# Performance work log

Hardware: AMD Instinct MI355X
Metric: run time of the kernel (lower is better)

## Reference

```python
import jax, jax.numpy as jnp
import numpy as np

NUM_HEADS = 8
POOL = 4  # kq_downscale kernel/stride (spatial)
B, S, H, W, C = 32, 8, 32, 32, 128
TOTAL_KEY_DEPTH = 512
VAL_FILTERS = 128
OUT_FILTERS = 64


def _avg_pool(x):
    # tf.nn.avg_pool3d with kernel/stride [1,1,4,4,1], SAME padding (dims divide evenly)
    win = (1, 1, POOL, POOL, 1)
    s = jax.lax.reduce_window(x, 0.0, jax.lax.add, win, win, 'SAME')
    return s / (POOL * POOL)


def _conv2d(x, w, b):
    # TimeDistributed Conv2D, same padding. x: (B,S,H,W,Cin), w: (kh,kw,Cin,Cout)
    Bx, Sx, Hx, Wx, Cx = x.shape
    y = jax.lax.conv_general_dilated(
        x.reshape(Bx * Sx, Hx, Wx, Cx), w, (1, 1), 'SAME',
        dimension_numbers=('NHWC', 'HWIO', 'NHWC'))
    return y.reshape(Bx, Sx, Hx, Wx, -1) + b


def _rel_emb(length_q, length_k, max_rel, table):
    # _generate_relative_positions_embeddings
    rk = jnp.arange(length_k)
    rq = rk[-length_q:]
    idx = jnp.clip(rk[None, :] - rq[:, None], -max_rel, max_rel) + max_rel
    return table[idx]  # (Lq, Lk, depth)


def setup_inputs() -> dict:
    key = jax.random.key(0)
    ks = jax.random.split(key, 11)
    qk_in = (H // POOL) * (W // POOL) * C          # 8*8*128 = 8192
    d_vh = H * W * VAL_FILTERS // NUM_HEADS         # 16384 per-head value depth
    d_kh = TOTAL_KEY_DEPTH // NUM_HEADS             # 64
    return {
        'inputs': jax.random.normal(ks[0], (B, 1, H, W, C), jnp.float32),
        'k_antecedent': jax.random.normal(ks[1], (B, S, H, W, C), jnp.float32),
        'v_antecedent': jax.random.normal(ks[2], (B, S, H, W, C), jnp.float32),
        'w_q': jax.random.normal(ks[3], (qk_in, TOTAL_KEY_DEPTH), jnp.float32) * 0.02,
        'w_k': jax.random.normal(ks[4], (qk_in, TOTAL_KEY_DEPTH), jnp.float32) * 0.02,
        'conv_v_w': jax.random.normal(ks[5], (3, 3, C, VAL_FILTERS), jnp.float32) * 0.02,
        'conv_v_b': jnp.zeros((VAL_FILTERS,), jnp.float32),
        'conv_o_w': jax.random.normal(ks[6], (3, 3, VAL_FILTERS, OUT_FILTERS), jnp.float32) * 0.02,
        'conv_o_b': jnp.zeros((OUT_FILTERS,), jnp.float32),
        'table_k': jax.random.normal(ks[7], (S, d_kh), jnp.float32) * 0.05,
        'table_v': jax.random.normal(ks[8], (S, d_vh), jnp.float32) * 0.05,
    }


def reference(inputs, k_antecedent, v_antecedent, w_q, w_k,
              conv_v_w, conv_v_b, conv_o_w, conv_o_b, table_k, table_v):
    Bx, Sx, Hx, Wx, Cx = v_antecedent.shape
    nh = NUM_HEADS
    max_rel = Sx // 2 - 1  # attn_factor_reduc/2 - 1

    # downscale + flatten q/k antecedents
    q_a = _avg_pool(inputs).reshape(Bx, 1, -1)
    k_a = _avg_pool(k_antecedent).reshape(Bx, Sx, -1)
    q = q_a @ w_q                   # (B,1,Dk)
    k = k_a @ w_k                   # (B,S,Dk)
    v = _conv2d(v_antecedent, conv_v_w, conv_v_b).reshape(Bx, Sx, -1)  # (B,S,Dv)

    def split(x):  # (B,L,D) -> (B,h,L,D/h)
        Bz, L, D = x.shape
        return x.reshape(Bz, L, nh, D // nh).transpose(0, 2, 1, 3)

    q, k, v = split(q), split(k), split(v)
    q = q * (q.shape[-1] ** -0.5)

    # relative-position logits: _relative_attention_inner(q, k, z_k, transpose=True)
    z_k = _rel_emb(1, Sx, max_rel, table_k)  # (1,S,dkh)
    logits = jnp.einsum('bhqd,bhkd->bhqk', q, k) + jnp.einsum('bhqd,qkd->bhqk', q, z_k)
    weights = jax.nn.softmax(logits, axis=-1)  # (B,h,1,S)

    # relative values: _relative_attention_inner(weights, v, z_v, transpose=False)
    z_v = _rel_emb(1, Sx, max_rel, table_v)  # (1,S,dvh)
    x = jnp.einsum('bhqk,bhkd->bhqd', weights, v) + jnp.einsum('bhqk,qkd->bhqd', weights, z_v)

    # combine heads, restore spatial shape, output conv
    x = x.transpose(0, 2, 1, 3).reshape(Bx, 1, Hx, Wx, -1)  # (B,1,H,W,Fv)
    out = _conv2d(x, conv_o_w, conv_o_b)                     # (B,1,H,W,Fo)
    return out
```

## Files before the change

kernel.cpp:

```cpp
#include <hip/hip_runtime.h>
#include <hip/hip_bf16.h>

typedef __hip_bfloat16 bf16;
typedef __attribute__((ext_vector_type(8))) short bf16x8;
typedef __attribute__((ext_vector_type(4))) float f32x4;

constexpr int B_ = 32, S_ = 8, H_ = 32, W_ = 32, C_ = 128;
constexpr int NH_ = 8, KD_ = 512, DKH_ = 64, VF_ = 128, OF_ = 64;
constexpr int QKIN_ = 8192;

static __device__ __forceinline__ short bfbits(float f) {
    bf16 h = __float2bfloat16(f);
    short s;
    __builtin_memcpy(&s, &h, 2);
    return s;
}
static __device__ __forceinline__ unsigned int packbf2(float a, float b) {
    return ((unsigned int)(unsigned short)bfbits(b) << 16) | (unsigned short)bfbits(a);
}


static __device__ __forceinline__ void dev_pool4(const float* __restrict__ in,
                                                 short* __restrict__ out, int idx) {
    int c4 = (idx & 31) * 4;
    int pw = (idx >> 5) & 7;
    int ph = (idx >> 8) & 7;
    int img = idx >> 11;
    const float* p = in + (((size_t)img * H_ + ph * 4) * W_ + pw * 4) * C_ + c4;
    float4 s = {0.f, 0.f, 0.f, 0.f};
#pragma unroll
    for (int dy = 0; dy < 4; ++dy)
#pragma unroll
        for (int dx = 0; dx < 4; ++dx) {
            float4 v = *reinterpret_cast<const float4*>(p + (dy * W_ + dx) * C_);
            s.x += v.x; s.y += v.y; s.z += v.z; s.w += v.w;
        }
    uint2 pk;
    pk.x = packbf2(s.x * 0.0625f, s.y * 0.0625f);
    pk.y = packbf2(s.z * 0.0625f, s.w * 0.0625f);
    *reinterpret_cast<uint2*>(out + (size_t)img * QKIN_ + (ph * 8 + pw) * 128 + c4) = pk;
}

static __device__ __forceinline__ void dev_wT(const float* __restrict__ w,
                                              short* __restrict__ wT, int local,
                                              float (*t)[65]) {
    int k0 = (local >> 3) * 64, n0 = (local & 7) * 64;
    int col = threadIdx.x & 63, r4 = threadIdx.x >> 6;
#pragma unroll
    for (int i = 0; i < 16; ++i) {
        int kr = i * 4 + r4;
        t[kr][col] = w[(size_t)(k0 + kr) * KD_ + n0 + col];
    }
    __syncthreads();
    int n = threadIdx.x >> 3, kg = threadIdx.x & 7;
#pragma unroll
    for (int half = 0; half < 2; ++half) {
        int nn = n + half * 32;
        short v[8];
#pragma unroll
        for (int j = 0; j < 8; ++j) v[j] = bfbits(t[kg * 8 + j][nn]);
        *reinterpret_cast<bf16x8*>(wT + (size_t)(n0 + nn) * QKIN_ + k0 + kg * 8) =
            *reinterpret_cast<bf16x8*>(v);
    }
}

static __device__ __forceinline__ void dev_wtrans(const float* __restrict__ in,
                                                  short* __restrict__ out, int idx,
                                                  int CO) {
    int tap = idx / (128 * CO);
    int rem = idx % (128 * CO);
    int co = rem / 128;
    int ci = rem & 127;
    out[idx] = bfbits(in[((size_t)tap * 128 + ci) * CO + co]);
}

constexpr int PB_ZERO  = 144;
constexpr int PB_POOLI = PB_ZERO + 256;
constexpr int PB_POOLK = PB_POOLI + 2048;
constexpr int PB_WTQ   = PB_POOLK + 1024;
constexpr int PB_WTK   = PB_WTQ + 1024;
constexpr int PB_WV    = PB_WTK + 576;
constexpr int PB_WO    = PB_WV + 288;

__global__ __launch_bounds__(256) void k_prep(
    const float* __restrict__ inp, const float* __restrict__ k_ant,
    const float* __restrict__ w_q, const float* __restrict__ w_k,
    const float* __restrict__ cvw, const float* __restrict__ cow,
    float* __restrict__ qk_zero, short* __restrict__ q_a, short* __restrict__ k_a,
    short* __restrict__ wqT, short* __restrict__ wkT,
    short* __restrict__ wvT, short* __restrict__ woT) {
    __shared__ float t[64][65];
    int bx = blockIdx.x;
    if (bx < PB_ZERO) {
        int i = (bx * 256 + threadIdx.x) * 4;
        float4 z = {0.f, 0.f, 0.f, 0.f};
        *reinterpret_cast<float4*>(qk_zero + i) = z;
    } else if (bx < PB_POOLI) {
        dev_pool4(inp, q_a, (bx - PB_ZERO) * 256 + threadIdx.x);
    } else if (bx < PB_POOLK) {
        dev_pool4(k_ant, k_a, (bx - PB_POOLI) * 256 + threadIdx.x);
    } else if (bx < PB_WTK) {
        if (bx < PB_WTQ)
            dev_wT(w_q, wqT, bx - PB_POOLK, t);
        else
            dev_wT(w_k, wkT, bx - PB_WTQ, t);
    } else if (bx < PB_WV) {
        dev_wtrans(cvw, wvT, (bx - PB_WTK) * 256 + threadIdx.x, 128);
    } else {
        dev_wtrans(cow, woT, (bx - PB_WV) * 256 + threadIdx.x, 64);
    }
}

__global__ __launch_bounds__(256) void k_gemm2(
    const short* __restrict__ qa, const short* __restrict__ ka,
    const short* __restrict__ wqTp, const short* __restrict__ wkTp,
    float* __restrict__ qo, float* __restrict__ ko) {
    int wave = threadIdx.x >> 6, lane = threadIdx.x & 63;
    int quad = lane >> 4, l15 = lane & 15;
    int id = blockIdx.x;
    const short* A;
    const short* WT;
    float* out;
    int m0, rem;
    if (id < 64) {
        A = qa; WT = wqTp; out = qo; m0 = 0; rem = id;
    } else {
        id -= 64;
        A = ka; WT = wkTp; out = ko;
        m0 = (id >> 6) * 32; rem = id & 63;
    }
    int n0 = (rem & 3) * 128 + wave * 32;
    int k0 = (rem >> 2) * 512;
    f32x4 acc[2][2];
#pragma unroll
    for (int mt = 0; mt < 2; ++mt)
#pragma unroll
        for (int nt = 0; nt < 2; ++nt) acc[mt][nt] = (f32x4){0.f, 0.f, 0.f, 0.f};
    const short* a0p = A + (size_t)(m0 + l15) * QKIN_;
    const short* a1p = a0p + 16 * QKIN_;
    const short* b0p = WT + (size_t)(n0 + l15) * QKIN_;
    const short* b1p = b0p + 16 * QKIN_;
    for (int kk = k0 + quad * 8; kk < k0 + 512; kk += 32) {
        bf16x8 a0 = *reinterpret_cast<const bf16x8*>(a0p + kk);
        bf16x8 a1 = *reinterpret_cast<const bf16x8*>(a1p + kk);
        bf16x8 b0 = *reinterpret_cast<const bf16x8*>(b0p + kk);
        bf16x8 b1 = *reinterpret_cast<const bf16x8*>(b1p + kk);
        acc[0][0] = __builtin_amdgcn_mfma_f32_16x16x32_bf16(a0, b0, acc[0][0], 0, 0, 0);
        acc[0][1] = __builtin_amdgcn_mfma_f32_16x16x32_bf16(a0, b1, acc[0][1], 0, 0, 0);
        acc[1][0] = __builtin_amdgcn_mfma_f32_16x16x32_bf16(a1, b0, acc[1][0], 0, 0, 0);
        acc[1][1] = __builtin_amdgcn_mfma_f32_16x16x32_bf16(a1, b1, acc[1][1], 0, 0, 0);
    }
#pragma unroll
    for (int mt = 0; mt < 2; ++mt)
#pragma unroll
        for (int nt = 0; nt < 2; ++nt)
#pragma unroll
            for (int reg = 0; reg < 4; ++reg)
                atomicAdd(&out[(size_t)(m0 + mt * 16 + quad * 4 + reg) * KD_ +
                               n0 + nt * 16 + l15],
                          acc[mt][nt][reg]);
}

__global__ __launch_bounds__(256) void k_convv_mfma(
    const float* __restrict__ v_ant, const short* __restrict__ wvT,
    const float* __restrict__ bias, const float* __restrict__ tbv,
    const float* __restrict__ q, const float* __restrict__ kmat,
    const float* __restrict__ tbk, short* __restrict__ x) {
    __shared__ short strip[6 * 34 * 136];
    __shared__ float w8s[8];
    int b = blockIdx.x >> 3, h = blockIdx.x & 7;
    int y0 = 4 * h;
    if (threadIdx.x < 64) {
        int d = threadIdx.x;
        float qv = q[(size_t)b * KD_ + h * DKH_ + d];
        float lg[8];
        float m = -1e30f;
#pragma unroll
        for (int s = 0; s < 8; ++s) {
            int zi = (s < 4) ? 0 : (s - 4);
            float kv = kmat[((size_t)b * S_ + s) * KD_ + h * DKH_ + d] + tbk[zi * DKH_ + d];
            float p = qv * kv * 0.125f;
#pragma unroll
            for (int msk = 1; msk < 64; msk <<= 1) p += __shfl_xor(p, msk);
            lg[s] = p;
            m = fmaxf(m, p);
        }
        float sum = 0.f;
#pragma unroll
        for (int s = 0; s < 8; ++s) {
            lg[s] = expf(lg[s] - m);
            sum += lg[s];
        }
        if (d == 0) {
            float inv = 1.f / sum;
#pragma unroll
            for (int s = 0; s < 8; ++s) w8s[s] = lg[s] * inv;
        }
    }
    for (int i = threadIdx.x; i < 384; i += 256) {
        int r = i >> 6, remz = i & 63;
        int side = remz >> 5, cg = remz & 31;
        uint2 z = {0u, 0u};
        *reinterpret_cast<uint2*>(&strip[(r * 34 + side * 33) * 136 + cg * 4]) = z;
    }
    __syncthreads();
    float w8[8];
#pragma unroll
    for (int kk = 0; kk < 8; ++kk) w8[kk] = w8s[kk];
    for (int i = threadIdx.x; i < 6 * 1024; i += 256) {
        int r = i >> 10, rem = i & 1023;
        int yimg = y0 - 1 + r;
        float4 s = {0.f, 0.f, 0.f, 0.f};
        if (0 <= yimg && yimg < H_) {
            const float* base = v_ant + (size_t)b * 1048576 + yimg * 4096 + rem * 4;
#pragma unroll
            for (int kk = 0; kk < 8; ++kk) {
                float4 v = *reinterpret_cast<const float4*>(base + (size_t)kk * 131072);
                s.x = fmaf(w8[kk], v.x, s.x);
                s.y = fmaf(w8[kk], v.y, s.y);
                s.z = fmaf(w8[kk], v.z, s.z);
                s.w = fmaf(w8[kk], v.w, s.w);
            }
        }
        int px = rem >> 5, cg = rem & 31;
        uint2 pk;
        pk.x = packbf2(s.x, s.y);
        pk.y = packbf2(s.z, s.w);
        *reinterpret_cast<uint2*>(&strip[(r * 34 + px + 1) * 136 + cg * 4]) = pk;
    }
    __syncthreads();
    int wave = threadIdx.x >> 6, lane = threadIdx.x & 63;
    int quad = lane >> 4, l15 = lane & 15;
    int n0 = wave * 32;
    f32x4 acc[8][2];
#pragma unroll
    for (int mt = 0; mt < 8; ++mt)
#pragma unroll
        for (int nt = 0; nt < 2; ++nt) acc[mt][nt] = (f32x4){0.f, 0.f, 0.f, 0.f};
    for (int kc = 0; kc < 36; ++kc) {
        int tap = kc >> 2;
        int ci0 = (kc & 3) * 32 + quad * 8;
        int ky = tap / 3, dx = tap % 3;
        bf16x8 bfr[2];
#pragma unroll
        for (int nt = 0; nt < 2; ++nt) {
            int co = n0 + nt * 16 + l15;
            bfr[nt] = *reinterpret_cast<const bf16x8*>(
                wvT + ((size_t)tap * 128 + co) * 128 + ci0);
        }
#pragma unroll
        for (int mt = 0; mt < 8; ++mt) {
            int jout = mt >> 1, half = mt & 1;
            int r = jout + ky;
            int px1 = half * 16 + l15 + dx;
            bf16x8 afr = *reinterpret_cast<const bf16x8*>(
                &strip[(r * 34 + px1) * 136 + ci0]);
            acc[mt][0] = __builtin_amdgcn_mfma_f32_16x16x32_bf16(afr, bfr[0], acc[mt][0], 0, 0, 0);
            acc[mt][1] = __builtin_amdgcn_mfma_f32_16x16x32_bf16(afr, bfr[1], acc[mt][1], 0, 0, 0);
        }
    }
    float cw[4];
    cw[0] = w8[0] + w8[1] + w8[2] + w8[3] + w8[4];
    cw[1] = w8[5];
    cw[2] = w8[6];
    cw[3] = w8[7];
#pragma unroll
    for (int mt = 0; mt < 8; ++mt) {
        int jout = mt >> 1, half = mt & 1;
#pragma unroll
        for (int nt = 0; nt < 2; ++nt) {
            int co = n0 + nt * 16 + l15;
            float bv = bias[co];
#pragma unroll
            for (int reg = 0; reg < 4; ++reg) {
                int px = half * 16 + quad * 4 + reg;
                int d = jout * 4096 + px * 128 + co;
                float v = acc[mt][nt][reg] + bv;
                v = fmaf(cw[0], tbv[d], v);
                v = fmaf(cw[1], tbv[16384 + d], v);
                v = fmaf(cw[2], tbv[32768 + d], v);
                v = fmaf(cw[3], tbv[49152 + d], v);
                x[(((size_t)b * H_ + y0 + jout) * W_ + px) * C_ + co] = bfbits(v);
            }
        }
    }
}

__global__ __launch_bounds__(256) void k_convo_mfma(
    const short* __restrict__ x, const short* __restrict__ woT,
    const float* __restrict__ bias, float* __restrict__ out) {
    __shared__ short strip[6 * 34 * 136];
    int b = blockIdx.x >> 3, rg = blockIdx.x & 7;
    int y0 = 4 * rg;
    for (int i = threadIdx.x; i < 384; i += 256) {
        int r = i >> 6, remz = i & 63;
        int side = remz >> 5, cg = remz & 31;
        uint2 z = {0u, 0u};
        *reinterpret_cast<uint2*>(&strip[(r * 34 + side * 33) * 136 + cg * 4]) = z;
    }
    for (int i = threadIdx.x; i < 6 * 1024; i += 256) {
        int r = i >> 10, rem = i & 1023;
        int yimg = y0 - 1 + r;
        uint2 v = {0u, 0u};
        if (0 <= yimg && yimg < H_)
            v = *reinterpret_cast<const uint2*>(
                x + (size_t)b * 131072 + yimg * 4096 + rem * 4);
        int px = rem >> 5, cg = rem & 31;
        *reinterpret_cast<uint2*>(&strip[(r * 34 + px + 1) * 136 + cg * 4]) = v;
    }
    __syncthreads();
    int wave = threadIdx.x >> 6, lane = threadIdx.x & 63;
    int quad = lane >> 4, l15 = lane & 15;
    int co = wave * 16 + l15;
    f32x4 acc[8];
#pragma unroll
    for (int mt = 0; mt < 8; ++mt) acc[mt] = (f32x4){0.f, 0.f, 0.f, 0.f};
    for (int kc = 0; kc < 36; ++kc) {
        int tap = kc >> 2;
        int ci0 = (kc & 3) * 32 + quad * 8;
        int ky = tap / 3, dx = tap % 3;
        bf16x8 bfr = *reinterpret_cast<const bf16x8*>(
            woT + ((size_t)tap * 64 + co) * 128 + ci0);
#pragma unroll
        for (int mt = 0; mt < 8; ++mt) {
            int jout = mt >> 1, half = mt & 1;
            int r = jout + ky;
            int px1 = half * 16 + l15 + dx;
            bf16x8 afr = *reinterpret_cast<const bf16x8*>(
                &strip[(r * 34 + px1) * 136 + ci0]);
            acc[mt] = __builtin_amdgcn_mfma_f32_16x16x32_bf16(afr, bfr, acc[mt], 0, 0, 0);
        }
    }
    float bv = bias[co];
#pragma unroll
    for (int mt = 0; mt < 8; ++mt) {
        int jout = mt >> 1, half = mt & 1;
#pragma unroll
        for (int reg = 0; reg < 4; ++reg) {
            int px = half * 16 + quad * 4 + reg;
            out[(((size_t)b * H_ + y0 + jout) * W_ + px) * OF_ + co] = acc[mt][reg] + bv;
        }
    }
}

extern "C" void kernel_launch(void* const* d_in, const int* in_sizes, int n_in,
                              void* d_out, int out_size, void* d_ws, size_t ws_size,
                              hipStream_t stream) {
    const float* inp   = (const float*)d_in[0];
    const float* k_ant = (const float*)d_in[1];
    const float* v_ant = (const float*)d_in[2];
    const float* w_q   = (const float*)d_in[3];
    const float* w_k   = (const float*)d_in[4];
    const float* cvw   = (const float*)d_in[5];
    const float* cvb   = (const float*)d_in[6];
    const float* cow   = (const float*)d_in[7];
    const float* cob   = (const float*)d_in[8];
    const float* tbk   = (const float*)d_in[9];
    const float* tbv   = (const float*)d_in[10];

    char* wsb = (char*)d_ws;
    float* q    = (float*)(wsb + 0);
    float* k    = (float*)(wsb + 65536);
    short* q_a  = (short*)(wsb + 598016);
    short* k_a  = (short*)(wsb + 1122304);
    short* wvT  = (short*)(wsb + 5316608);
    short* woT  = (short*)(wsb + 5611520);
    short* wkT  = (short*)(wsb + 5758976);
    short* wqT  = (short*)(wsb + 14147584);
    short* x    = wqT;

    k_prep<<<PB_WO, 256, 0, stream>>>(inp, k_ant, w_q, w_k, cvw, cow,
                                      q, q_a, k_a, wqT, wkT, wvT, woT);
    k_gemm2<<<576, 256, 0, stream>>>(q_a, k_a, wqT, wkT, q, k);
    k_convv_mfma<<<256, 256, 0, stream>>>(v_ant, wvT, cvb, tbv, q, k, tbk, x);
    k_convo_mfma<<<256, 256, 0, stream>>>(x, woT, cob, (float*)d_out);
}
```

Baseline: 400.6 us.

## Split softmax-weighted value mixing into a separate wide-grid kernel before conv

The weighted sum over the 8 time steps of v_antecedent moves out of the conv kernel into a new k_mix kernel launched with 1536 blocks. The memory-bound read of the large value tensor is therefore spread across many more blocks than the 256-block conv kernel had. The conv kernel then stages precomputed bf16 halo strips, with loads batched to raise memory-level parallelism, and weight transpose and pooling loads are vectorized or batched. The cost is an extra launch, a workspace round trip for the mixed tensor (including duplicated halo rows), and the softmax being computed redundantly in both kernels.

New measurement: 402.7 us. Within noise of the previous version (+0.5%).

```diff
diff --git a/kernel.cpp b/kernel.cpp
--- a/kernel.cpp
+++ b/kernel.cpp
@@ -29,12 +29,18 @@
     const float* p = in + (((size_t)img * H_ + ph * 4) * W_ + pw * 4) * C_ + c4;
     float4 s = {0.f, 0.f, 0.f, 0.f};
 #pragma unroll
-    for (int dy = 0; dy < 4; ++dy)
-#pragma unroll
-        for (int dx = 0; dx < 4; ++dx) {
-            float4 v = *reinterpret_cast<const float4*>(p + (dy * W_ + dx) * C_);
-            s.x += v.x; s.y += v.y; s.z += v.z; s.w += v.w;
-        }
+    for (int half = 0; half < 2; ++half) {
+        float4 v[8];
+#pragma unroll
+        for (int j = 0; j < 8; ++j) {
+            int dy = half * 2 + (j >> 2), dx = j & 3;
+            v[j] = *reinterpret_cast<const float4*>(p + (dy * W_ + dx) * C_);
+        }
+#pragma unroll
+        for (int j = 0; j < 8; ++j) {
+            s.x += v[j].x; s.y += v[j].y; s.z += v[j].z; s.w += v[j].w;
+        }
+    }
     uint2 pk;
     pk.x = packbf2(s.x * 0.0625f, s.y * 0.0625f);
     pk.y = packbf2(s.z * 0.0625f, s.w * 0.0625f);
@@ -45,11 +51,16 @@
                                               short* __restrict__ wT, int local,
                                               float (*t)[65]) {
     int k0 = (local >> 3) * 64, n0 = (local & 7) * 64;
-    int col = threadIdx.x & 63, r4 = threadIdx.x >> 6;
-#pragma unroll
-    for (int i = 0; i < 16; ++i) {
-        int kr = i * 4 + r4;
-        t[kr][col] = w[(size_t)(k0 + kr) * KD_ + n0 + col];
+    int c4 = (threadIdx.x & 15) * 4, r16 = threadIdx.x >> 4;
+#pragma unroll
+    for (int i = 0; i < 4; ++i) {
+        int kr = i * 16 + r16;
+        float4 v = *reinterpret_cast<const float4*>(
+            w + (size_t)(k0 + kr) * KD_ + n0 + c4);
+        t[kr][c4 + 0] = v.x;
+        t[kr][c4 + 1] = v.y;
+        t[kr][c4 + 2] = v.z;
+        t[kr][c4 + 3] = v.w;
     }
     __syncthreads();
     int n = threadIdx.x >> 3, kg = threadIdx.x & 7;
@@ -161,8 +172,144 @@
                           acc[mt][nt][reg]);
 }
 
-__global__ __launch_bounds__(256) void k_convv_mfma(
-    const float* __restrict__ v_ant, const short* __restrict__ wvT,
+static __device__ __forceinline__ void dev_softmax(
+    const float* __restrict__ q, const float* __restrict__ kmat,
+    const float* __restrict__ tbk, int b, int h, float* w8s) {
+    if (threadIdx.x < 64) {
+        int d = threadIdx.x;
+        float qv = q[(size_t)b * KD_ + h * DKH_ + d];
+        float lg[8];
+        float m = -1e30f;
+#pragma unroll
+        for (int s = 0; s < 8; ++s) {
+            int zi = (s < 4) ? 0 : (s - 4);
+            float kv = kmat[((size_t)b * S_ + s) * KD_ + h * DKH_ + d] + tbk[zi * DKH_ + d];
+            float p = qv * kv * 0.125f;
+#pragma unroll
+            for (int msk = 1; msk < 64; msk <<= 1) p += __shfl_xor(p, msk);
+            lg[s] = p;
+            m = fmaxf(m, p);
+        }
+        float sum = 0.f;
+#pragma unroll
+        for (int s = 0; s < 8; ++s) {
+            lg[s] = expf(lg[s] - m);
+            sum += lg[s];
+        }
+        if (d == 0) {
+            float inv = 1.f / sum;
+#pragma unroll
+            for (int s = 0; s < 8; ++s) w8s[s] = lg[s] * inv;
+        }
+    }
+}
+
+__global__ __launch_bounds__(256) void k_mix(
+    const float* __restrict__ v_ant, const float* __restrict__ q,
+    const float* __restrict__ kmat, const float* __restrict__ tbk,
+    short* __restrict__ xmix) {
+    __shared__ float w8s[8];
+    int bx = blockIdx.x;
+    int b = bx / 48;
+    int rem6 = bx % 48;
+    int h = rem6 / 6, r = rem6 % 6;
+    dev_softmax(q, kmat, tbk, b, h, w8s);
+    __syncthreads();
+    int yimg = 4 * h - 1 + r;
+    short* outp = xmix + ((size_t)(b * 8 + h) * 6 + r) * 4096;
+    if (yimg < 0 || yimg >= H_) {
+        uint2 z = {0u, 0u};
+#pragma unroll
+        for (int it = 0; it < 4; ++it) {
+            int off = (it * 256 + threadIdx.x) * 4;
+            *reinterpret_cast<uint2*>(outp + off) = z;
+        }
+        return;
+    }
+    float w8[8];
+#pragma unroll
+    for (int s = 0; s < 8; ++s) w8[s] = w8s[s];
+    const float* base0 = v_ant + (size_t)b * 1048576 + yimg * 4096;
+#pragma unroll
+    for (int it = 0; it < 4; ++it) {
+        int off = (it * 256 + threadIdx.x) * 4;
+        float4 v[8];
+#pragma unroll
+        for (int s = 0; s < 8; ++s)
+            v[s] = *reinterpret_cast<const float4*>(base0 + (size_t)s * 131072 + off);
+        float4 a = {0.f, 0.f, 0.f, 0.f};
+#pragma unroll
+        for (int s = 0; s < 8; ++s) {
+            a.x = fmaf(w8[s], v[s].x, a.x);
+            a.y = fmaf(w8[s], v[s].y, a.y);
+            a.z = fmaf(w8[s], v[s].z, a.z);
+            a.w = fmaf(w8[s], v[s].w, a.w);
+        }
+        uint2 pk;
+        pk.x = packbf2(a.x, a.y);
+        pk.y = packbf2(a.z, a.w);
+        *reinterpret_cast<uint2*>(outp + off) = pk;
+    }
+}
+
+static __device__ __forceinline__ void dev_stage_copy(const short* __restrict__ src,
+                                                      short* __restrict__ strip) {
+    for (int i = threadIdx.x; i < 384; i += 256) {
+        int r = i >> 6, remz = i & 63;
+        int side = remz >> 5, cg = remz & 31;
+        uint2 z = {0u, 0u};
+        *reinterpret_cast<uint2*>(&strip[(r * 34 + side * 33) * 136 + cg * 4]) = z;
+    }
+#pragma unroll
+    for (int round = 0; round < 3; ++round) {
+        uint2 vv[8];
+#pragma unroll
+        for (int j = 0; j < 8; ++j) {
+            int i = (round * 8 + j) * 256 + threadIdx.x;
+            vv[j] = *reinterpret_cast<const uint2*>(src + i * 4);
+        }
+#pragma unroll
+        for (int j = 0; j < 8; ++j) {
+            int i = (round * 8 + j) * 256 + threadIdx.x;
+            int r = i >> 10, rem = i & 1023;
+            int px = rem >> 5, cg = rem & 31;
+            *reinterpret_cast<uint2*>(&strip[(r * 34 + px + 1) * 136 + cg * 4]) = vv[j];
+        }
+    }
+}
+
+static __device__ __forceinline__ void dev_stage6(const short* __restrict__ src,
+                                                  int y0, short* __restrict__ strip) {
+    for (int i = threadIdx.x; i < 384; i += 256) {
+        int r = i >> 6, remz = i & 63;
+        int side = remz >> 5, cg = remz & 31;
+        uint2 z = {0u, 0u};
+        *reinterpret_cast<uint2*>(&strip[(r * 34 + side * 33) * 136 + cg * 4]) = z;
+    }
+#pragma unroll
+    for (int round = 0; round < 3; ++round) {
+        uint2 vv[8];
+#pragma unroll
+        for (int j = 0; j < 8; ++j) {
+            int i = (round * 8 + j) * 256 + threadIdx.x;
+            int r = i >> 10, rem = i & 1023;
+            int yimg = y0 - 1 + r;
+            vv[j] = (uint2){0u, 0u};
+            if (0 <= yimg && yimg < H_)
+                vv[j] = *reinterpret_cast<const uint2*>(src + yimg * 4096 + rem * 4);
+        }
+#pragma unroll
+        for (int j = 0; j < 8; ++j) {
+            int i = (round * 8 + j) * 256 + threadIdx.x;
+            int r = i >> 10, rem = i & 1023;
+            int px = rem >> 5, cg = rem & 31;
+            *reinterpret_cast<uint2*>(&strip[(r * 34 + px + 1) * 136 + cg * 4]) = vv[j];
+        }
+    }
+}
+
+__global__ __launch_bounds__(256) void k_convv2(
+    const short* __restrict__ xmix, const short* __restrict__ wvT,
     const float* __restrict__ bias, const float* __restrict__ tbv,
     const float* __restrict__ q, const float* __restrict__ kmat,
     const float* __restrict__ tbk, short* __restrict__ x) {
@@ -170,64 +317,8 @@
     __shared__ float w8s[8];
     int b = blockIdx.x >> 3, h = blockIdx.x & 7;
     int y0 = 4 * h;
-    if (threadIdx.x < 64) {
-        int d = threadIdx.x;
-        float qv = q[(size_t)b * KD_ + h * DKH_ + d];
-        float lg[8];
-        float m = -1e30f;
-#pragma unroll
-        for (int s = 0; s < 8; ++s) {
-            int zi = (s < 4) ? 0 : (s - 4);
-            float kv = kmat[((size_t)b * S_ + s) * KD_ + h * DKH_ + d] + tbk[zi * DKH_ + d];
-            float p = qv * kv * 0.125f;
-#pragma unroll
-            for (int msk = 1; msk < 64; msk <<= 1) p += __shfl_xor(p, msk);
-            lg[s] = p;
-            m = fmaxf(m, p);
-        }
-        float sum = 0.f;
-#pragma unroll
-        for (int s = 0; s < 8; ++s) {
-            lg[s] = expf(lg[s] - m);
-            sum += lg[s];
-        }
-        if (d == 0) {
-            float inv = 1.f / sum;
-#pragma unroll
-            for (int s = 0; s < 8; ++s) w8s[s] = lg[s] * inv;
-        }
-    }
-    for (int i = threadIdx.x; i < 384; i += 256) {
-        int r = i >> 6, remz = i & 63;
-        int side = remz >> 5, cg = remz & 31;
-        uint2 z = {0u, 0u};
-        *reinterpret_cast<uint2*>(&strip[(r * 34 + side * 33) * 136 + cg * 4]) = z;
-    }
-    __syncthreads();
-    float w8[8];
-#pragma unroll
-    for (int kk = 0; kk < 8; ++kk) w8[kk] = w8s[kk];
-    for (int i = threadIdx.x; i < 6 * 1024; i += 256) {
-        int r = i >> 10, rem = i & 1023;
-        int yimg = y0 - 1 + r;
-        float4 s = {0.f, 0.f, 0.f, 0.f};
-        if (0 <= yimg && yimg < H_) {
-            const float* base = v_ant + (size_t)b * 1048576 + yimg * 4096 + rem * 4;
-#pragma unroll
-            for (int kk = 0; kk < 8; ++kk) {
-                float4 v = *reinterpret_cast<const float4*>(base + (size_t)kk * 131072);
-                s.x = fmaf(w8[kk], v.x, s.x);
-                s.y = fmaf(w8[kk], v.y, s.y);
-                s.z = fmaf(w8[kk], v.z, s.z);
-                s.w = fmaf(w8[kk], v.w, s.w);
-            }
-        }
-        int px = rem >> 5, cg = rem & 31;
-        uint2 pk;
-        pk.x = packbf2(s.x, s.y);
-        pk.y = packbf2(s.z, s.w);
-        *reinterpret_cast<uint2*>(&strip[(r * 34 + px + 1) * 136 + cg * 4]) = pk;
-    }
+    dev_softmax(q, kmat, tbk, b, h, w8s);
+    dev_stage_copy(xmix + (size_t)(b * 8 + h) * 6 * 4096, strip);
     __syncthreads();
     int wave = threadIdx.x >> 6, lane = threadIdx.x & 63;
     int quad = lane >> 4, l15 = lane & 15;
@@ -260,10 +351,10 @@
         }
     }
     float cw[4];
-    cw[0] = w8[0] + w8[1] + w8[2] + w8[3] + w8[4];
-    cw[1] = w8[5];
-    cw[2] = w8[6];
-    cw[3] = w8[7];
+    cw[0] = w8s[0] + w8s[1] + w8s[2] + w8s[3] + w8s[4];
+    cw[1] = w8s[5];
+    cw[2] = w8s[6];
+    cw[3] = w8s[7];
 #pragma unroll
     for (int mt = 0; mt < 8; ++mt) {
         int jout = mt >> 1, half = mt & 1;
@@ -292,22 +383,7 @@
     __shared__ short strip[6 * 34 * 136];
     int b = blockIdx.x >> 3, rg = blockIdx.x & 7;
     int y0 = 4 * rg;
-    for (int i = threadIdx.x; i < 384; i += 256) {
-        int r = i >> 6, remz = i & 63;
-        int side = remz >> 5, cg = remz & 31;
-        uint2 z = {0u, 0u};
-        *reinterpret_cast<uint2*>(&strip[(r * 34 + side * 33) * 136 + cg * 4]) = z;
-    }
-    for (int i = threadIdx.x; i < 6 * 1024; i += 256) {
-        int r = i >> 10, rem = i & 1023;
-        int yimg = y0 - 1 + r;
-        uint2 v = {0u, 0u};
-        if (0 <= yimg && yimg < H_)
-            v = *reinterpret_cast<const uint2*>(
-                x + (size_t)b * 131072 + yimg * 4096 + rem * 4);
-        int px = rem >> 5, cg = rem & 31;
-        *reinterpret_cast<uint2*>(&strip[(r * 34 + px + 1) * 136 + cg * 4]) = v;
-    }
+    dev_stage6(x + (size_t)b * 131072, y0, strip);
     __syncthreads();
     int wave = threadIdx.x >> 6, lane = threadIdx.x & 63;
     int quad = lane >> 4, l15 = lane & 15;
@@ -367,11 +443,13 @@
     short* woT  = (short*)(wsb + 5611520);
     short* wkT  = (short*)(wsb + 5758976);
     short* wqT  = (short*)(wsb + 14147584);
-    short* x    = wqT;
+    short* xmix = (short*)(wsb + 22536192);
+    short* x    = wkT;
 
     k_prep<<<PB_WO, 256, 0, stream>>>(inp, k_ant, w_q, w_k, cvw, cow,
                                       q, q_a, k_a, wqT, wkT, wvT, woT);
     k_gemm2<<<576, 256, 0, stream>>>(q_a, k_a, wqT, wkT, q, k);
-    k_convv_mfma<<<256, 256, 0, stream>>>(v_ant, wvT, cvb, tbv, q, k, tbk, x);
+    k_mix<<<1536, 256, 0, stream>>>(v_ant, q, k, tbk, xmix);
+    k_convv2<<<256, 256, 0, stream>>>(xmix, wvT, cvb, tbv, q, k, tbk, x);
     k_convo_mfma<<<256, 256, 0, stream>>>(x, woT, cob, (float*)d_out);
 }
```
